# Kernel tuning notes

Hardware: AMD Instinct MI355X
Metric: run time of the kernel (lower is better)

## Reference

```python
import jax, jax.numpy as jnp
import numpy as np

SPS = 16
SPAN = 8
BETA = 0.5


def design_rrc(sps, span, beta):
    """Root-raised-cosine FIR taps, unit energy, shape (K,) float32."""
    num_taps = sps * span
    t = np.arange(num_taps) - (num_taps - 1) / 2
    ts = t / sps
    with np.errstate(divide='ignore', invalid='ignore'):
        num = np.sin(np.pi * ts * (1 - beta)) + 4 * beta * ts * np.cos(np.pi * ts * (1 + beta))
        den = np.pi * ts * (1 - (4 * beta * ts) ** 2)
        rrc = num / den
    rrc[np.isnan(rrc)] = 1.0
    energy = np.sum(rrc ** 2)
    if energy > 1e-15:
        rrc = rrc / np.sqrt(energy)
    return jnp.asarray(rrc, dtype=jnp.float32)


def setup_inputs() -> dict:
    key = jax.random.key(0)
    bits = jax.random.randint(key, (256, 16384), 0, 2, dtype=jnp.int32)
    rrc = design_rrc(SPS, SPAN, BETA)  # (128,)
    return {"bits": bits, "rrc": rrc}


def reference(bits, rrc):
    sps = SPS
    B, num_bits = bits.shape
    ns = num_bits // 2
    b2 = bits.reshape(B, ns, 2)
    # Gray map: (0,0)->(+1+1j), (0,1)->(-1+1j), (1,1)->(-1-1j), (1,0)->(+1-1j), /sqrt(2)
    inv_sqrt2 = jnp.float32(1.0 / np.sqrt(2.0))
    re = (1 - 2 * b2[..., 1]).astype(jnp.float32) * inv_sqrt2  # (B, ns)
    im = (1 - 2 * b2[..., 0]).astype(jnp.float32) * inv_sqrt2  # (B, ns)
    sym = jnp.stack([re, im], axis=1)  # (B, 2, ns) channels = [real, imag]

    up_len = ns * sps
    offset = sps // 2
    # zero-stuff upsample with half-sps right shift (pad-left-then-truncate in original)
    up = jnp.zeros((B, 2, up_len), jnp.float32).at[:, :, offset::sps].set(sym)

    K = rrc.shape[0]
    pad_l = (K - 1) // 2
    pad_r = K - 1 - pad_l
    kern = jnp.broadcast_to(rrc[None, None, :], (2, 1, K))  # depthwise, same taps for I/Q
    y = jax.lax.conv_general_dilated(
        up, kern, window_strides=(1,), padding=[(pad_l, pad_r)],
        feature_group_count=2)  # (B, 2, up_len), cross-correlation like torch conv1d
    y = y * jnp.float32(np.sqrt(sps))
    return jnp.transpose(y, (0, 2, 1))  # (B, up_len, 2) = [real, imag]
```

## Files before the change

### kernel.cpp

```cpp
#include <hip/hip_runtime.h>

#define SPS    16
#define NS     8192
#define NBITS  16384
#define UPLEN  (NS * SPS)
#define KTAPS  128
#define QPB    256
#define SWIN   264

typedef float vfloat4 __attribute__((ext_vector_type(4)));

__global__ __launch_bounds__(256, 4)
void qpsk_mod_kernel(const int* __restrict__ bits,
                     const float* __restrict__ rrc,
                     float* __restrict__ out) {
    __shared__ float s_taps[KTAPS];
    __shared__ float s_re[SWIN];
    __shared__ float s_im[SWIN];

    const int tid = threadIdx.x;
    const int b   = blockIdx.x >> 5;
    const int q0  = (blockIdx.x & 31) * QPB;

    if (tid < KTAPS) s_taps[tid] = rrc[tid];

    const float scale = 2.82842712474619f;
    for (int ls = tid; ls < SWIN; ls += 256) {
        int s = q0 - 4 + ls;
        float re = 0.f, im = 0.f;
        if (s >= 0 && s < NS) {
            int2 bb = *(const int2*)(bits + b * NBITS + 2 * s);
            re = (float)(1 - 2 * bb.y) * scale;
            im = (float)(1 - 2 * bb.x) * scale;
        }
        s_re[ls] = re;
        s_im[ls] = im;
    }
    __syncthreads();

    const int k   = tid & 7;
    const int gg  = tid >> 3;
    const int off = (k < 4) ? (6 - 2 * k) : (22 - 2 * k);
    const int sel = (k >= 4) ? 1 : 0;

    float tlo[8], thi[8];
#pragma unroll
    for (int i = 0; i < 8; ++i) {
        float2 tp = *(const float2*)(&s_taps[16 * i + off]);
        tlo[i] = tp.x;
        thi[i] = tp.y;
    }

    float* outp = out + (size_t)b * (UPLEN * 2)
                      + (size_t)q0 * 32 + (size_t)gg * 32 + 4 * k;

#pragma unroll
    for (int G = 0; G < 8; ++G) {
        const int wbase = G * 32 + gg + sel;
        float a0 = 0.f, a1 = 0.f, a2 = 0.f, a3 = 0.f;
#pragma unroll
        for (int i = 0; i < 8; ++i) {
            float sr = s_re[wbase + i];
            float si = s_im[wbase + i];
            a0 += thi[i] * sr;
            a1 += thi[i] * si;
            a2 += tlo[i] * sr;
            a3 += tlo[i] * si;
        }
        vfloat4 v = {a0, a1, a2, a3};
        __builtin_nontemporal_store(v, (vfloat4*)(outp + G * (32 * 32)));
    }
}

extern "C" void kernel_launch(void* const* d_in, const int* in_sizes, int n_in,
                              void* d_out, int out_size, void* d_ws, size_t ws_size,
                              hipStream_t stream) {
    const int*   bits = (const int*)d_in[0];
    const float* rrc  = (const float*)d_in[1];
    float*       out  = (float*)d_out;

    const int B = in_sizes[0] / NBITS;
    dim3 grid(B * (NS / QPB));
    qpsk_mod_kernel<<<grid, 256, 0, stream>>>(bits, rrc, out);
}
```

Measured before the change: 274.7 us.

## Compute four output samples per thread with interleaved symbol LDS layout

```diff
diff --git a/kernel.cpp b/kernel.cpp
--- a/kernel.cpp
+++ b/kernel.cpp
@@ -9,14 +9,14 @@
 #define SWIN   264
 
 typedef float vfloat4 __attribute__((ext_vector_type(4)));
+typedef float vfloat2 __attribute__((ext_vector_type(2)));
 
 __global__ __launch_bounds__(256, 4)
 void qpsk_mod_kernel(const int* __restrict__ bits,
                      const float* __restrict__ rrc,
                      float* __restrict__ out) {
-    __shared__ float s_taps[KTAPS];
-    __shared__ float s_re[SWIN];
-    __shared__ float s_im[SWIN];
+    __shared__ __align__(16) float s_taps[KTAPS];
+    __shared__ vfloat2 s_sym[SWIN];
 
     const int tid = threadIdx.x;
     const int b   = blockIdx.x >> 5;
@@ -27,48 +27,48 @@
     const float scale = 2.82842712474619f;
     for (int ls = tid; ls < SWIN; ls += 256) {
         int s = q0 - 4 + ls;
-        float re = 0.f, im = 0.f;
+        vfloat2 v = {0.f, 0.f};
         if (s >= 0 && s < NS) {
             int2 bb = *(const int2*)(bits + b * NBITS + 2 * s);
-            re = (float)(1 - 2 * bb.y) * scale;
-            im = (float)(1 - 2 * bb.x) * scale;
+            v.x = (float)(1 - 2 * bb.y) * scale;
+            v.y = (float)(1 - 2 * bb.x) * scale;
         }
-        s_re[ls] = re;
-        s_im[ls] = im;
+        s_sym[ls] = v;
     }
     __syncthreads();
 
-    const int k   = tid & 7;
-    const int gg  = tid >> 3;
-    const int off = (k < 4) ? (6 - 2 * k) : (22 - 2 * k);
-    const int sel = (k >= 4) ? 1 : 0;
+    const int k    = tid & 3;
+    const int gg   = tid >> 2;
+    const int base = (k < 2) ? (4 - 4 * k) : (20 - 4 * k);
+    const int sel  = (k >= 2) ? 1 : 0;
 
-    float tlo[8], thi[8];
+    vfloat4 t4[8];
 #pragma unroll
-    for (int i = 0; i < 8; ++i) {
-        float2 tp = *(const float2*)(&s_taps[16 * i + off]);
-        tlo[i] = tp.x;
-        thi[i] = tp.y;
-    }
+    for (int i = 0; i < 8; ++i)
+        t4[i] = *(const vfloat4*)(&s_taps[16 * i + base]);
 
     float* outp = out + (size_t)b * (UPLEN * 2)
-                      + (size_t)q0 * 32 + (size_t)gg * 32 + 4 * k;
+                      + (size_t)(q0 + gg) * 32 + 8 * k;
 
 #pragma unroll
-    for (int G = 0; G < 8; ++G) {
-        const int wbase = G * 32 + gg + sel;
+    for (int G = 0; G < 4; ++G) {
+        const int wbase = G * 64 + gg + sel;
         float a0 = 0.f, a1 = 0.f, a2 = 0.f, a3 = 0.f;
+        float a4 = 0.f, a5 = 0.f, a6 = 0.f, a7 = 0.f;
 #pragma unroll
         for (int i = 0; i < 8; ++i) {
-            float sr = s_re[wbase + i];
-            float si = s_im[wbase + i];
-            a0 += thi[i] * sr;
-            a1 += thi[i] * si;
-            a2 += tlo[i] * sr;
-            a3 += tlo[i] * si;
+            vfloat2 s = s_sym[wbase + i];
+            vfloat4 t = t4[i];
+            a0 += t.w * s.x;  a1 += t.w * s.y;
+            a2 += t.z * s.x;  a3 += t.z * s.y;
+            a4 += t.y * s.x;  a5 += t.y * s.y;
+            a6 += t.x * s.x;  a7 += t.x * s.y;
         }
-        vfloat4 v = {a0, a1, a2, a3};
-        __builtin_nontemporal_store(v, (vfloat4*)(outp + G * (32 * 32)));
+        vfloat4 v0 = {a0, a1, a2, a3};
+        vfloat4 v1 = {a4, a5, a6, a7};
+        float* p = outp + (size_t)G * 2048;
+        __builtin_nontemporal_store(v0, (vfloat4*)p);
+        __builtin_nontemporal_store(v1, (vfloat4*)(p + 4));
     }
 }
 
```

New measurement: 333.3 us. +21.3%, slower.
